# Optimization experiments

Measured on AMD Instinct MI355X. Metric: run time of the kernel, lower is better.

## Reference

```python
import jax, jax.numpy as jnp
import numpy as np

W = 128
POS_FREQ = 10  # -> 3*10*2 = 60 encoded dims
VIEW_FREQ = 4  # -> 3*4*2 = 24 encoded dims


def freq_encode(v, n_freq):
    # tcnn 'Frequency' encoding: sin/cos of 2^j * pi * x per input dim.
    scales = (2.0 ** jnp.arange(n_freq, dtype=v.dtype)) * jnp.pi  # [F]
    ang = v[..., :, None] * scales  # [N, 3, F]
    enc = jnp.stack([jnp.sin(ang), jnp.cos(ang)], axis=-1)  # [N, 3, F, 2]
    return enc.reshape(v.shape[0], -1)  # [N, 3*F*2]


def mlp(h, weights):
    # tcnn FullyFusedMLP: bias-free, ReLU on hidden layers, linear output.
    for Wm in weights[:-1]:
        h = jax.nn.relu(h @ Wm)
    return h @ weights[-1]


def setup_inputs():
    key = jax.random.key(0)
    ks = jax.random.split(key, 10)
    N = 1048576

    def w(k, fan_in, fan_out):
        s = (1.0 / np.sqrt(fan_in)).astype(np.float32)
        return jax.random.uniform(k, (fan_in, fan_out), jnp.float32, -s, s)

    return {
        "x": jax.random.uniform(ks[0], (N, 6), jnp.float32),
        "Wd1_0": w(ks[1], 60, W),
        "Wd1_1": w(ks[2], W, W),
        "Wd1_2": w(ks[3], W, W),
        "Wd2_0": w(ks[4], 60 + W, W),
        "Wd2_1": w(ks[5], W, W),
        "Wd2_2": w(ks[6], W, W),
        "Wd2_3": w(ks[7], W, W + 1),
        "Wc_0": w(ks[8], 24 + W, W),
        "Wc_1": w(ks[9], W, 3),
    }


def reference(x, Wd1_0, Wd1_1, Wd1_2, Wd2_0, Wd2_1, Wd2_2, Wd2_3, Wc_0, Wc_1):
    pos, view = x[:, :3], x[:, 3:6]
    # Density MLP
    enc_pos = freq_encode(pos, POS_FREQ)                # [N, 60]
    part1 = mlp(enc_pos, [Wd1_0, Wd1_1, Wd1_2])          # [N, 128]
    dens_out = mlp(jnp.concatenate([enc_pos, part1], -1),
                   [Wd2_0, Wd2_1, Wd2_2, Wd2_3])         # [N, 129]
    blending = jax.nn.sigmoid(dens_out[:, :1])           # [N, 1]
    feature = dens_out[:, 1:]                            # [N, 128]
    density = feature[:, 0:1]                            # [N, 1]
    # Color MLP
    enc_view = freq_encode(view, VIEW_FREQ)              # [N, 24]
    rgb = mlp(jnp.concatenate([enc_view, feature], -1), [Wc_0, Wc_1])  # [N, 3]
    return jnp.concatenate([rgb, density, blending], -1)  # [N, 5]
```

## Files before the change

### kernel.cpp

```cpp
#include <hip/hip_runtime.h>
#include <cstdint>
#include <cstddef>

typedef __attribute__((ext_vector_type(8))) __bf16 bf16x8;
typedef __attribute__((ext_vector_type(16))) float floatx16;

struct SrcPtrs { const float* p[9]; };


__global__ void prep_zero(unsigned short* __restrict__ ws) {
  uint4* p = (uint4*)ws;
  const int n = 143360 / 8;
  for (int i = blockIdx.x * blockDim.x + threadIdx.x; i < n; i += gridDim.x * blockDim.x)
    p[i] = make_uint4(0u, 0u, 0u, 0u);
}

__global__ void prep_fill(SrcPtrs sp, unsigned short* __restrict__ ws) {
  const int m  = blockIdx.x >> 4;
  const int sl = blockIdx.x & 15;
  const int K[9]  = {60, 128, 128, 188, 128, 128, 128, 152, 128};
  const int N[9]  = {128, 128, 128, 128, 128, 128, 129, 128, 3};
  const int SS[9] = {4, 8, 8, 12, 8, 8, 8, 10, 8};
  const unsigned OFF[9] = {0u, 8192u, 24576u, 40960u, 65536u, 81920u, 98304u, 118784u, 139264u};
  const int Km = K[m], Nm = N[m], Sm = SS[m];
  const float* __restrict__ src = sp.p[m];
  unsigned short* __restrict__ dst = ws + OFF[m];
  const int tot = Km * Nm;
  for (int i = sl * 256 + (int)threadIdx.x; i < tot; i += 16 * 256) {
    int k = i / Nm;
    int n = i - k * Nm;
    int kk = k, row = n;
    if (m == 3) kk = (k < 60) ? 128 + k : k - 60;
    if (m == 7) kk = (k < 24) ? 128 + k : k - 24;
    if (m == 6) row = (n == 0) ? 128 : n - 1;
    kk = (kk & ~12) | (((kk & 4) << 1) | ((kk & 8) >> 1));
    const int t = row >> 5, l31 = row & 31;
    const int s = kk >> 4, q2 = (kk >> 3) & 1, j = kk & 7;
    dst[(t * Sm + s) * 512 + (q2 * 32 + l31) * 8 + j] =
        __builtin_bit_cast(unsigned short, (__bf16)src[i]);
  }
}


__device__ __forceinline__ unsigned pk2(float a, float b) {
  unsigned short ua = __builtin_bit_cast(unsigned short, (__bf16)a);
  unsigned short ub = __builtin_bit_cast(unsigned short, (__bf16)b);
  return (unsigned)ua | ((unsigned)ub << 16);
}

__device__ __forceinline__ void stage16(const void* g, void* l) {
  __builtin_amdgcn_global_load_lds(
      (const __attribute__((address_space(1))) unsigned int*)g,
      (__attribute__((address_space(3))) unsigned int*)l, 16, 0, 0);
}

template <int KIND>
__device__ __forceinline__ bf16x8 trig_frag(const float (&x)[6], int q2, int sl) {
  bf16x8 r;
#pragma unroll
  for (int j = 0; j < 8; ++j) {
    const int kA = 16 * sl + j + (j >= 4 ? 4 : 0);
    const int kB = kA + 4;
    int dA, dB; float scA, scB; bool vA, vB;
    if (KIND == 0) {
      vA = kA < 60; vB = kB < 60;
      dA = kA / 20; dB = kB / 20;
      scA = (float)(1 << ((kA % 20) >> 1)) * 0.5f;
      scB = (float)(1 << ((kB % 20) >> 1)) * 0.5f;
    } else {
      vA = kA < 24; vB = kB < 24;
      dA = 3 + (kA >> 3); dB = 3 + (kB >> 3);
      scA = (float)(1 << ((kA & 7) >> 1)) * 0.5f;
      scB = (float)(1 << ((kB & 7) >> 1)) * 0.5f;
    }
    float v  = q2 ? x[dB] : x[dA];
    float sc = q2 ? scB : scA;
    bool ok  = q2 ? vB : vA;
    float rev = v * sc;
    float t = (j & 1) ? __builtin_amdgcn_cosf(rev) : __builtin_amdgcn_sinf(rev);
    r[j] = (__bf16)(ok ? t : 0.0f);
  }
  return r;
}

template <bool RELU, int OUTM>
__device__ __forceinline__ void store_tile(int t, const floatx16& am0, const floatx16& am1,
                                           uint4 (&pout)[2][8], float* __restrict__ out,
                                           int q2, int pt0, int pt1) {
  if (OUTM == 2) {
    if (q2 == 0) {
      float* o0 = out + (size_t)pt0 * 5;
      o0[0] = am0[0]; o0[1] = am0[1]; o0[2] = am0[2];
      float* o1 = out + (size_t)pt1 * 5;
      o1[0] = am1[0]; o1[1] = am1[1]; o1[2] = am1[2];
    }
  } else {
    if (OUTM == 0 || t < 4) {
#pragma unroll
      for (int gg = 0; gg < 4; ++gg) {
        float b0 = am0[4 * gg], b1 = am0[4 * gg + 1];
        float b2 = am0[4 * gg + 2], b3 = am0[4 * gg + 3];
        float c0 = am1[4 * gg], c1 = am1[4 * gg + 1];
        float c2 = am1[4 * gg + 2], c3 = am1[4 * gg + 3];
        if (RELU) {
          b0 = fmaxf(b0, 0.f); b1 = fmaxf(b1, 0.f);
          b2 = fmaxf(b2, 0.f); b3 = fmaxf(b3, 0.f);
          c0 = fmaxf(c0, 0.f); c1 = fmaxf(c1, 0.f);
          c2 = fmaxf(c2, 0.f); c3 = fmaxf(c3, 0.f);
        }
        if ((gg & 1) == 0) {
          pout[0][2 * t + (gg >> 1)].x = pk2(b0, b1);
          pout[0][2 * t + (gg >> 1)].y = pk2(b2, b3);
          pout[1][2 * t + (gg >> 1)].x = pk2(c0, c1);
          pout[1][2 * t + (gg >> 1)].y = pk2(c2, c3);
        } else {
          pout[0][2 * t + (gg >> 1)].z = pk2(b0, b1);
          pout[0][2 * t + (gg >> 1)].w = pk2(b2, b3);
          pout[1][2 * t + (gg >> 1)].z = pk2(c0, c1);
          pout[1][2 * t + (gg >> 1)].w = pk2(c2, c3);
        }
      }
    }
    if (OUTM == 1 && q2 == 0) {
      if (t == 0) {
        out[(size_t)pt0 * 5 + 3] = am0[0];
        out[(size_t)pt1 * 5 + 3] = am1[0];
      }
      if (t == 4) {
        out[(size_t)pt0 * 5 + 4] = 1.0f / (1.0f + __expf(-am0[0]));
        out[(size_t)pt1 * 5 + 4] = 1.0f / (1.0f + __expf(-am1[0]));
      }
    }
  }
}

template <int S, int SL, int NT, int HT, int PP, bool RELU, int OUTM, int NB>
__device__ __forceinline__ void run_layer(const unsigned short* __restrict__ wsrc,
                                          const unsigned short* __restrict__ nsrc,
                                          unsigned short* __restrict__ sWt,
                                          const uint4 (&pin)[2][8],
                                          uint4 (&pout)[2][8],
                                          const bf16x8 (&tail)[2][4],
                                          floatx16 ZACC,
                                          float* __restrict__ out, int base, int tid) {
  const int lane = tid & 63;
  const int w = tid >> 6;
  const int q2 = lane >> 5;
  const int l31 = lane & 31;
  const int pt0 = base + w * 64 + l31;
  const int pt1 = pt0 + 32;

  __syncthreads();

  if (NB > 0) {
    const uint4* __restrict__ s4 = (const uint4*)nsrc;
    uint4* __restrict__ dst = (uint4*)(sWt + (PP ^ 1) * 12288);
#pragma unroll
    for (int kI = 0; kI < NB / (16 * 256); ++kI) {
      const int i = kI * 256 + tid;
      stage16(s4 + i, dst + (i & ~63));
    }
  }

  const unsigned short* __restrict__ ldsbuf = sWt + PP * 12288;
  const uint4* __restrict__ wp = (const uint4*)wsrc;

  auto loadA = [&](int p) -> bf16x8 {
    const int t = p / S, s = p % S;
    if (t < HT) return *(const bf16x8*)&ldsbuf[(t * S + s) * 512 + lane * 8];
    return __builtin_bit_cast(bf16x8, wp[(t * S + s) * 64 + lane]);
  };

  constexpr int TOT = NT * S;
  constexpr int DEPTH = 6;
  bf16x8 win[DEPTH];

#pragma unroll
  for (int p = 0; p < DEPTH && p < TOT; ++p) win[p] = loadA(p);

  floatx16 a0, a1;
#pragma unroll
  for (int p = 0; p < TOT; ++p) {
    const int t = p / S, s = p % S;
    bf16x8 A = win[p % DEPTH];
    if (p + DEPTH < TOT) win[p % DEPTH] = loadA(p + DEPTH);
    bf16x8 B0 = (s < SL) ? __builtin_bit_cast(bf16x8, pin[0][(s < SL) ? s : 0])
                         : tail[0][s - SL];
    bf16x8 B1 = (s < SL) ? __builtin_bit_cast(bf16x8, pin[1][(s < SL) ? s : 0])
                         : tail[1][s - SL];
    if (s == 0) {
      a0 = __builtin_amdgcn_mfma_f32_32x32x16_bf16(A, B0, ZACC, 0, 0, 0);
      a1 = __builtin_amdgcn_mfma_f32_32x32x16_bf16(A, B1, ZACC, 0, 0, 0);
    } else {
      a0 = __builtin_amdgcn_mfma_f32_32x32x16_bf16(A, B0, a0, 0, 0, 0);
      a1 = __builtin_amdgcn_mfma_f32_32x32x16_bf16(A, B1, a1, 0, 0, 0);
    }
    if (s == S - 1)
      store_tile<RELU, OUTM>(t, a0, a1, pout, out, q2, pt0, pt1);
  }
}

__global__ __launch_bounds__(256, 2) void nerf_main(const float* __restrict__ x,
                                                    const unsigned short* __restrict__ ws,
                                                    float* __restrict__ out) {
  __shared__ __align__(16) unsigned short sWt[2 * 12288];

  const int tid = (int)threadIdx.x;
  const int base = (int)blockIdx.x * 256;
  const int lane = tid & 63;
  const int w = tid >> 6;
  const int q2 = lane >> 5;
  const int l31 = lane & 31;
  const int pt0 = base + w * 64 + l31;

  {
    const uint4* s4 = (const uint4*)ws;
    uint4* dst = (uint4*)sWt;
#pragma unroll
    for (int i = 0; i < 2; ++i)
      stage16(s4 + i * 256 + tid, dst + ((i * 256 + tid) & ~63));
  }

  float x0[6], x1[6];
  {
    const float* a = x + (size_t)pt0 * 6;
    const float* b = x + (size_t)(pt0 + 32) * 6;
#pragma unroll
    for (int c = 0; c < 3; ++c) {
      float2 u = *(const float2*)(a + 2 * c);
      float2 v = *(const float2*)(b + 2 * c);
      x0[2 * c] = u.x; x0[2 * c + 1] = u.y;
      x1[2 * c] = v.x; x1[2 * c + 1] = v.y;
    }
  }

  bf16x8 pkt[2][4];
#pragma unroll
  for (int sl = 0; sl < 4; ++sl) {
    pkt[0][sl] = trig_frag<0>(x0, q2, sl);
    pkt[1][sl] = trig_frag<0>(x1, q2, sl);
  }

  floatx16 zacc;
#pragma unroll
  for (int i = 0; i < 16; ++i) zacc[i] = 0.0f;

  uint4 P0[2][8], P1[2][8];

  run_layer< 4, 0, 4, 2, 0, true , 0, 16384>(ws + 0u,      ws + 8192u,   sWt, P0, P0, pkt, zacc, out, base, tid);
  run_layer< 8, 8, 4, 2, 1, true , 0, 16384>(ws + 8192u,   ws + 24576u,  sWt, P0, P1, pkt, zacc, out, base, tid);
  run_layer< 8, 8, 4, 2, 0, false, 0, 24576>(ws + 24576u,  ws + 40960u,  sWt, P1, P0, pkt, zacc, out, base, tid);
  run_layer<12, 8, 4, 2, 1, true , 0, 16384>(ws + 40960u,  ws + 65536u,  sWt, P0, P1, pkt, zacc, out, base, tid);
  run_layer< 8, 8, 4, 2, 0, true , 0, 16384>(ws + 65536u,  ws + 81920u,  sWt, P1, P0, pkt, zacc, out, base, tid);
  run_layer< 8, 8, 4, 2, 1, true , 0, 24576>(ws + 81920u,  ws + 98304u,  sWt, P0, P1, pkt, zacc, out, base, tid);
  run_layer< 8, 8, 5, 3, 0, false, 1, 20480>(ws + 98304u,  ws + 118784u, sWt, P1, P0, pkt, zacc, out, base, tid);

  bf16x8 vw[2][4];
#pragma unroll
  for (int sl = 0; sl < 2; ++sl) {
    vw[0][sl] = trig_frag<1>(x0, q2, sl);
    vw[1][sl] = trig_frag<1>(x1, q2, sl);
  }
  vw[0][2] = vw[0][0]; vw[0][3] = vw[0][0];
  vw[1][2] = vw[1][0]; vw[1][3] = vw[1][0];

  run_layer<10, 8, 4, 2, 1, true , 0,  8192>(ws + 118784u, ws + 139264u, sWt, P0, P1, vw,  zacc, out, base, tid);
  run_layer< 8, 8, 1, 1, 0, false, 2,     0>(ws + 139264u, (const unsigned short*)nullptr, sWt, P1, P0, pkt, zacc, out, base, tid);
}

extern "C" void kernel_launch(void* const* d_in, const int* in_sizes, int n_in,
                              void* d_out, int out_size, void* d_ws, size_t ws_size,
                              hipStream_t stream) {
  (void)n_in; (void)out_size; (void)ws_size;
  const float* x = (const float*)d_in[0];
  SrcPtrs sp;
  for (int i = 0; i < 9; ++i) sp.p[i] = (const float*)d_in[1 + i];
  unsigned short* ws = (unsigned short*)d_ws;
  float* out = (float*)d_out;
  const int N = in_sizes[0] / 6;

  prep_zero<<<70, 256, 0, stream>>>(ws);
  prep_fill<<<144, 256, 0, stream>>>(sp, ws);
  nerf_main<<<N / 256, 256, 0, stream>>>(x, ws, out);
}
```

Before: 349.5 us.

## Drop LDS weight staging and read all weight fragments directly from global memory

After: 361.5 us. +3.4%, slower.

```diff
diff --git a/kernel.cpp b/kernel.cpp
--- a/kernel.cpp
+++ b/kernel.cpp
@@ -48,12 +48,6 @@
   return (unsigned)ua | ((unsigned)ub << 16);
 }
 
-__device__ __forceinline__ void stage16(const void* g, void* l) {
-  __builtin_amdgcn_global_load_lds(
-      (const __attribute__((address_space(1))) unsigned int*)g,
-      (__attribute__((address_space(3))) unsigned int*)l, 16, 0, 0);
-}
-
 template <int KIND>
 __device__ __forceinline__ bf16x8 trig_frag(const float (&x)[6], int q2, int sl) {
   bf16x8 r;
@@ -134,10 +128,8 @@
   }
 }
 
-template <int S, int SL, int NT, int HT, int PP, bool RELU, int OUTM, int NB>
+template <int S, int SL, int NT, bool RELU, int OUTM>
 __device__ __forceinline__ void run_layer(const unsigned short* __restrict__ wsrc,
-                                          const unsigned short* __restrict__ nsrc,
-                                          unsigned short* __restrict__ sWt,
                                           const uint4 (&pin)[2][8],
                                           uint4 (&pout)[2][8],
                                           const bf16x8 (&tail)[2][4],
@@ -150,40 +142,23 @@
   const int pt0 = base + w * 64 + l31;
   const int pt1 = pt0 + 32;
 
-  __syncthreads();
-
-  if (NB > 0) {
-    const uint4* __restrict__ s4 = (const uint4*)nsrc;
-    uint4* __restrict__ dst = (uint4*)(sWt + (PP ^ 1) * 12288);
-#pragma unroll
-    for (int kI = 0; kI < NB / (16 * 256); ++kI) {
-      const int i = kI * 256 + tid;
-      stage16(s4 + i, dst + (i & ~63));
-    }
-  }
-
-  const unsigned short* __restrict__ ldsbuf = sWt + PP * 12288;
   const uint4* __restrict__ wp = (const uint4*)wsrc;
 
-  auto loadA = [&](int p) -> bf16x8 {
-    const int t = p / S, s = p % S;
-    if (t < HT) return *(const bf16x8*)&ldsbuf[(t * S + s) * 512 + lane * 8];
-    return __builtin_bit_cast(bf16x8, wp[(t * S + s) * 64 + lane]);
-  };
-
   constexpr int TOT = NT * S;
-  constexpr int DEPTH = 6;
+  constexpr int DEPTH = 8;
   bf16x8 win[DEPTH];
 
 #pragma unroll
-  for (int p = 0; p < DEPTH && p < TOT; ++p) win[p] = loadA(p);
+  for (int p = 0; p < DEPTH && p < TOT; ++p)
+    win[p] = __builtin_bit_cast(bf16x8, wp[p * 64 + lane]);
 
   floatx16 a0, a1;
 #pragma unroll
   for (int p = 0; p < TOT; ++p) {
     const int t = p / S, s = p % S;
     bf16x8 A = win[p % DEPTH];
-    if (p + DEPTH < TOT) win[p % DEPTH] = loadA(p + DEPTH);
+    if (p + DEPTH < TOT)
+      win[p % DEPTH] = __builtin_bit_cast(bf16x8, wp[(p + DEPTH) * 64 + lane]);
     bf16x8 B0 = (s < SL) ? __builtin_bit_cast(bf16x8, pin[0][(s < SL) ? s : 0])
                          : tail[0][s - SL];
     bf16x8 B1 = (s < SL) ? __builtin_bit_cast(bf16x8, pin[1][(s < SL) ? s : 0])
@@ -203,8 +178,6 @@
 __global__ __launch_bounds__(256, 2) void nerf_main(const float* __restrict__ x,
                                                     const unsigned short* __restrict__ ws,
                                                     float* __restrict__ out) {
-  __shared__ __align__(16) unsigned short sWt[2 * 12288];
-
   const int tid = (int)threadIdx.x;
   const int base = (int)blockIdx.x * 256;
   const int lane = tid & 63;
@@ -213,14 +186,6 @@
   const int l31 = lane & 31;
   const int pt0 = base + w * 64 + l31;
 
-  {
-    const uint4* s4 = (const uint4*)ws;
-    uint4* dst = (uint4*)sWt;
-#pragma unroll
-    for (int i = 0; i < 2; ++i)
-      stage16(s4 + i * 256 + tid, dst + ((i * 256 + tid) & ~63));
-  }
-
   float x0[6], x1[6];
   {
     const float* a = x + (size_t)pt0 * 6;
@@ -247,13 +212,13 @@
 
   uint4 P0[2][8], P1[2][8];
 
-  run_layer< 4, 0, 4, 2, 0, true , 0, 16384>(ws + 0u,      ws + 8192u,   sWt, P0, P0, pkt, zacc, out, base, tid);
-  run_layer< 8, 8, 4, 2, 1, true , 0, 16384>(ws + 8192u,   ws + 24576u,  sWt, P0, P1, pkt, zacc, out, base, tid);
-  run_layer< 8, 8, 4, 2, 0, false, 0, 24576>(ws + 24576u,  ws + 40960u,  sWt, P1, P0, pkt, zacc, out, base, tid);
-  run_layer<12, 8, 4, 2, 1, true , 0, 16384>(ws + 40960u,  ws + 65536u,  sWt, P0, P1, pkt, zacc, out, base, tid);
-  run_layer< 8, 8, 4, 2, 0, true , 0, 16384>(ws + 65536u,  ws + 81920u,  sWt, P1, P0, pkt, zacc, out, base, tid);
-  run_layer< 8, 8, 4, 2, 1, true , 0, 24576>(ws + 81920u,  ws + 98304u,  sWt, P0, P1, pkt, zacc, out, base, tid);
-  run_layer< 8, 8, 5, 3, 0, false, 1, 20480>(ws + 98304u,  ws + 118784u, sWt, P1, P0, pkt, zacc, out, base, tid);
+  run_layer< 4, 0, 4, true , 0>(ws + 0u,      P0, P0, pkt, zacc, out, base, tid);
+  run_layer< 8, 8, 4, true , 0>(ws + 8192u,   P0, P1, pkt, zacc, out, base, tid);
+  run_layer< 8, 8, 4, false, 0>(ws + 24576u,  P1, P0, pkt, zacc, out, base, tid);
+  run_layer<12, 8, 4, true , 0>(ws + 40960u,  P0, P1, pkt, zacc, out, base, tid);
+  run_layer< 8, 8, 4, true , 0>(ws + 65536u,  P1, P0, pkt, zacc, out, base, tid);
+  run_layer< 8, 8, 4, true , 0>(ws + 81920u,  P0, P1, pkt, zacc, out, base, tid);
+  run_layer< 8, 8, 5, false, 1>(ws + 98304u,  P1, P0, pkt, zacc, out, base, tid);
 
   bf16x8 vw[2][4];
 #pragma unroll
@@ -264,8 +229,8 @@
   vw[0][2] = vw[0][0]; vw[0][3] = vw[0][0];
   vw[1][2] = vw[1][0]; vw[1][3] = vw[1][0];
 
-  run_layer<10, 8, 4, 2, 1, true , 0,  8192>(ws + 118784u, ws + 139264u, sWt, P0, P1, vw,  zacc, out, base, tid);
-  run_layer< 8, 8, 1, 1, 0, false, 2,     0>(ws + 139264u, (const unsigned short*)nullptr, sWt, P1, P0, pkt, zacc, out, base, tid);
+  run_layer<10, 8, 4, true , 0>(ws + 118784u, P0, P1, vw,  zacc, out, base, tid);
+  run_layer< 8, 8, 1, false, 2>(ws + 139264u, P1, P0, pkt, zacc, out, base, tid);
 }
 
 extern "C" void kernel_launch(void* const* d_in, const int* in_sizes, int n_in,
```
